# Kernel tuning notes

Measured on AMD Instinct MI355X. Metric: run time of the kernel, lower is better.

The kernel has to match this reference:

```python
import jax, jax.numpy as jnp
import numpy as np

B = 64            # batch of graphs
E = 8978          # edge-simplices per graph (nodes of the Hodge-1 graph)
E2 = E // 2       # after Graclus pair-pooling
K = 4             # Laguerre polynomial order
DEG = 16          # avg degree of the (edge-)adjacency
SLOPE = 0.33      # LeakyReLU negative slope
EPS = 1e-5        # BatchNorm eps


def _make_edges(rng, b, n, deg):
    # block-diagonal batched edge list: each graph only connects within itself
    offs = np.repeat(np.arange(b, dtype=np.int64) * n, n * deg)
    dst = np.tile(np.repeat(np.arange(n, dtype=np.int64), deg), b) + offs
    src = rng.integers(0, n, size=b * n * deg) + offs
    return np.stack([src, dst]).astype(np.int32)


def setup_inputs() -> dict:
    rng = np.random.default_rng(0)
    ks = jax.random.split(jax.random.key(0), 12)
    N1 = B * E
    ei1 = _make_edges(rng, B, E, DEG)
    ei2 = _make_edges(rng, B, E2, DEG)
    return {
        "x_s": jax.random.normal(ks[0], (N1, 1), jnp.float32),
        "edge_index_s": jnp.asarray(ei1),
        "edge_weight_s": jax.random.uniform(ks[1], (ei1.shape[1],), jnp.float32) * (2.0 / DEG),
        "edge_index_s1": jnp.asarray(ei2),
        "edge_weight_s1": jax.random.uniform(ks[2], (ei2.shape[1],), jnp.float32) * (2.0 / DEG),
        "W0": jax.random.normal(ks[3], (K, 1, 32), jnp.float32) * 0.3,
        "b0": jnp.zeros((32,), jnp.float32),
        "g0": jnp.ones((32,), jnp.float32),
        "be0": jnp.zeros((32,), jnp.float32),
        "W1": jax.random.normal(ks[4], (K, 32, 32), jnp.float32) * 0.1,
        "b1": jnp.zeros((32,), jnp.float32),
        "g1": jnp.ones((32,), jnp.float32),
        "be1": jnp.zeros((32,), jnp.float32),
        "W2": jax.random.normal(ks[5], (K, 32, 1), jnp.float32) * 0.1,
        "b2": jnp.zeros((1,), jnp.float32),
        "g2": jnp.ones((1,), jnp.float32),
        "be2": jnp.zeros((1,), jnp.float32),
        "lin1_W": jax.random.normal(ks[6], (E2, 256), jnp.float32) * 0.02,
        "lin1_b": jnp.zeros((256,), jnp.float32),
        "bn1_g": jnp.ones((256,), jnp.float32),
        "bn1_b": jnp.zeros((256,), jnp.float32),
        "lin2_W": jax.random.normal(ks[7], (256, 128), jnp.float32) * 0.06,
        "lin2_b": jnp.zeros((128,), jnp.float32),
        "bn2_g": jnp.ones((128,), jnp.float32),
        "bn2_b": jnp.zeros((128,), jnp.float32),
        "lin3_W": jax.random.normal(ks[8], (128, 1), jnp.float32) * 0.09,
        "lin3_b": jnp.zeros((1,), jnp.float32),
    }


def _laguerre_layer(x, src, dst, ew, W, b, gamma, beta, n):
    """HodgeLaguerreConv (K-order Laguerre recurrence over sparse L) + BatchNorm + LeakyReLU."""
    def matvec(v):  # (L v)[i] = sum_j w_ij v[j]
        return jax.ops.segment_sum(ew[:, None] * v[src], dst, num_segments=n)
    Tp = x                      # L_0(L) x = x
    out = Tp @ W[0]
    Tc = x - matvec(x)          # L_1(L) x = x - L x
    out = out + Tc @ W[1]
    for k in range(1, K - 1):   # L_{k+1} = ((2k+1-L) L_k - k L_{k-1}) / (k+1)
        Tn = ((2 * k + 1) * Tc - matvec(Tc) - k * Tp) / (k + 1)
        out = out + Tn @ W[k + 1]
        Tp, Tc = Tc, Tn
    out = out + b
    out = gamma * (out - out.mean(0)) * jax.lax.rsqrt(out.var(0) + EPS) + beta
    return jnp.where(out > 0, out, SLOPE * out)


def _bn(h, g, b):
    return g * (h - h.mean(0)) * jax.lax.rsqrt(h.var(0) + EPS) + b


def reference(x_s, edge_index_s, edge_weight_s, edge_index_s1, edge_weight_s1,
              W0, b0, g0, be0, W1, b1, g1, be1, W2, b2, g2, be2,
              lin1_W, lin1_b, bn1_g, bn1_b, lin2_W, lin2_b, bn2_g, bn2_b,
              lin3_W, lin3_b):
    N1, N2 = B * E, B * E2
    x = _laguerre_layer(x_s, edge_index_s[0], edge_index_s[1], edge_weight_s,
                        W0, b0, g0, be0, N1)
    # Graclus pooling: merge matched node pairs by max over features
    x = x.reshape(B, E2, 2, x.shape[-1]).max(axis=2).reshape(N2, -1)
    x = _laguerre_layer(x, edge_index_s1[0], edge_index_s1[1], edge_weight_s1,
                        W1, b1, g1, be1, N2)
    x = _laguerre_layer(x, edge_index_s1[0], edge_index_s1[1], edge_weight_s1,
                        W2, b2, g2, be2, N2)
    x = x.reshape(B, E2)        # last conv has 1 channel
    h = jax.nn.relu(_bn(x @ lin1_W + lin1_b, bn1_g, bn1_b))
    h = jax.nn.relu(_bn(h @ lin2_W + lin2_b, bn2_g, bn2_b))
    return h @ lin3_W + lin3_b  # [B, num_classes=1]
```

## Files before the change

kernel.cpp:

```cpp
#include <hip/hip_runtime.h>
#include <cstdint>

#define SLOPE 0.33f

static constexpr int B_   = 64;
static constexpr int E1_  = 8978;
static constexpr int E2_  = 4489;
static constexpr int N1_  = B_ * E1_;
static constexpr int N2_  = B_ * E2_;
static constexpr int DEG_ = 16;
static constexpr int SLC1_ = 1123;
static constexpr int SLC2_ = 562;
static constexpr double EPS_ = 1e-5;

typedef unsigned short u16;
typedef unsigned int   u32;

__device__ __forceinline__ float lrelu(float v) { return v > 0.f ? v : SLOPE * v; }
__device__ __forceinline__ float dot4(float4 a, float4 b) {
  return a.x * b.x + a.y * b.y + a.z * b.z + a.w * b.w;
}
__device__ __forceinline__ void gacc(float4& acc, float wgt, const float4& gv) {
  acc.x += wgt * gv.x; acc.y += wgt * gv.y; acc.z += wgt * gv.z; acc.w += wgt * gv.w;
}

template<int NPG>
__device__ __forceinline__ void comp_idx(const int* __restrict__ src, int node,
    u16* __restrict__ out) {
  int gbase = (node / NPG) * NPG;
  const int4* s4 = (const int4*)(src + (size_t)node * DEG_);
  int4 a = s4[0], b = s4[1], c = s4[2], d = s4[3];
  uint4 o0, o1;
  o0.x = (u32)(a.x - gbase) | ((u32)(a.y - gbase) << 16);
  o0.y = (u32)(a.z - gbase) | ((u32)(a.w - gbase) << 16);
  o0.z = (u32)(b.x - gbase) | ((u32)(b.y - gbase) << 16);
  o0.w = (u32)(b.z - gbase) | ((u32)(b.w - gbase) << 16);
  o1.x = (u32)(c.x - gbase) | ((u32)(c.y - gbase) << 16);
  o1.y = (u32)(c.z - gbase) | ((u32)(c.w - gbase) << 16);
  o1.z = (u32)(d.x - gbase) | ((u32)(d.y - gbase) << 16);
  o1.w = (u32)(d.z - gbase) | ((u32)(d.w - gbase) << 16);
  uint4* op = (uint4*)(out + (size_t)node * DEG_);
  op[0] = o0; op[1] = o1;
}

__global__ __launch_bounds__(256) void k_prep_all(const int* __restrict__ src1,
    const int* __restrict__ src2, const float* __restrict__ W1,
    u16* __restrict__ lsrc1, u16* __restrict__ lsrc2, float* __restrict__ qb) {
  int blk = blockIdx.x;
  if (blk < 2245) {
    int node = blk * 256 + threadIdx.x;
    if (node < N1_) comp_idx<E1_>(src1, node, lsrc1);
  } else if (blk < 3368) {
    int node = (blk - 2245) * 256 + threadIdx.x;
    if (node < N2_) comp_idx<E2_>(src2, node, lsrc2);
  } else {
    int idx = (blk - 3368) * 256 + threadIdx.x;
    if (idx < 4096) {
      int e = idx & 3, rr = (idx >> 2) & 3, qq = (idx >> 4) & 7, oq = idx >> 7;
      int j = oq >> 3, c = (oq & 7) * 4 + rr, in = 4 * qq + e;
      float k0, k1, k2, k3;
      if (j == 0)      { k0 = 0.f; k1 = 0.f; k2 = 0.f;  k3 = -1.f / 6.f; }
      else if (j == 1) { k0 = 0.f; k1 = 0.f; k2 = 0.5f; k3 = 1.5f; }
      else if (j == 2) { k0 = 0.f; k1 = -1.f; k2 = -2.f; k3 = -3.f; }
      else             { k0 = 1.f; k1 = 1.f; k2 = 1.f;  k3 = 1.f; }
      const float* wp = W1 + in * 32 + c;
      qb[idx] = k0 * wp[0] + k1 * wp[1024] + k2 * wp[2048] + k3 * wp[3072];
    }
  }
}

#define GATHER1(dst, sv, si_, w4_)                                              \
  {                                                                             \
    uint4 A_ = si_[0], Bq_ = si_[1];                                            \
    float4 w_;                                                                  \
    w_ = w4_[0];                                                                \
    dst += w_.x * sv[A_.x & 0xFFFFu] + w_.y * sv[A_.x >> 16]                    \
         + w_.z * sv[A_.y & 0xFFFFu] + w_.w * sv[A_.y >> 16];                   \
    w_ = w4_[1];                                                                \
    dst += w_.x * sv[A_.z & 0xFFFFu] + w_.y * sv[A_.z >> 16]                    \
         + w_.z * sv[A_.w & 0xFFFFu] + w_.w * sv[A_.w >> 16];                   \
    w_ = w4_[2];                                                                \
    dst += w_.x * sv[Bq_.x & 0xFFFFu] + w_.y * sv[Bq_.x >> 16]                  \
         + w_.z * sv[Bq_.y & 0xFFFFu] + w_.w * sv[Bq_.y >> 16];                 \
    w_ = w4_[3];                                                                \
    dst += w_.x * sv[Bq_.z & 0xFFFFu] + w_.y * sv[Bq_.z >> 16]                  \
         + w_.z * sv[Bq_.w & 0xFFFFu] + w_.w * sv[Bq_.w >> 16];                 \
  }

__global__ __launch_bounds__(512) void k0_mv1(const float* __restrict__ x,
    const u16* __restrict__ lsrc, const float* __restrict__ ew, float* __restrict__ T1) {
  __shared__ float sx[E1_];
  int g = blockIdx.x >> 3, q = blockIdx.x & 7;
  int gbase = g * E1_;
  for (int j = threadIdx.x; j < E1_; j += 512) sx[j] = x[gbase + j];
  __syncthreads();
  int start = q * SLC1_, end = min(start + SLC1_, E1_);
  for (int i = start + (int)threadIdx.x; i < end; i += 512) {
    int node = gbase + i;
    const uint4* si = (const uint4*)(lsrc + (size_t)node * DEG_);
    const float4* w4 = (const float4*)(ew + (size_t)node * DEG_);
    float acc = 0.f;
    GATHER1(acc, sx, si, w4);
    T1[node] = sx[i] - acc;
  }
}

__global__ __launch_bounds__(512) void k0_mv2(const float* __restrict__ x,
    const u16* __restrict__ lsrc, const float* __restrict__ ew,
    const float* __restrict__ T1, float* __restrict__ T2) {
  __shared__ float sT[E1_];
  int g = blockIdx.x >> 3, q = blockIdx.x & 7;
  int gbase = g * E1_;
  for (int j = threadIdx.x; j < E1_; j += 512) sT[j] = T1[gbase + j];
  __syncthreads();
  int start = q * SLC1_, end = min(start + SLC1_, E1_);
  for (int i = start + (int)threadIdx.x; i < end; i += 512) {
    int node = gbase + i;
    const uint4* si = (const uint4*)(lsrc + (size_t)node * DEG_);
    const float4* w4 = (const float4*)(ew + (size_t)node * DEG_);
    float acc = 0.f;
    GATHER1(acc, sT, si, w4);
    T2[node] = (3.f * sT[i] - acc - x[node]) * 0.5f;
  }
}

__global__ __launch_bounds__(512) void k0_mv3(const float* __restrict__ x,
    const u16* __restrict__ lsrc, const float* __restrict__ ew,
    const float* __restrict__ T1, const float* __restrict__ T2,
    float* __restrict__ T3, double* mom) {
  __shared__ float sT[E1_];
  __shared__ double sred[8 * 14];
  int g = blockIdx.x >> 3, q = blockIdx.x & 7;
  int gbase = g * E1_;
  for (int j = threadIdx.x; j < E1_; j += 512) sT[j] = T2[gbase + j];
  __syncthreads();
  double m[14];
#pragma unroll
  for (int j = 0; j < 14; ++j) m[j] = 0.0;
  int start = q * SLC1_, end = min(start + SLC1_, E1_);
  for (int i = start + (int)threadIdx.x; i < end; i += 512) {
    int node = gbase + i;
    const uint4* si = (const uint4*)(lsrc + (size_t)node * DEG_);
    const float4* w4 = (const float4*)(ew + (size_t)node * DEG_);
    float acc = 0.f;
    GATHER1(acc, sT, si, w4);
    float t1 = T1[node];
    float t2 = sT[i];
    float t3 = (5.f * t2 - acc - 2.f * t1) * (1.f / 3.f);
    T3[node] = t3;
    double d0 = x[node], d1 = t1, d2 = t2, d3 = t3;
    m[0] += d0; m[1] += d1; m[2] += d2; m[3] += d3;
    m[4] += d0 * d0; m[5] += d0 * d1; m[6] += d0 * d2; m[7] += d0 * d3;
    m[8] += d1 * d1; m[9] += d1 * d2; m[10] += d1 * d3;
    m[11] += d2 * d2; m[12] += d2 * d3; m[13] += d3 * d3;
  }
  int lane = threadIdx.x & 63, wid = threadIdx.x >> 6;
#pragma unroll
  for (int j = 0; j < 14; ++j) {
    double v = m[j];
    for (int o = 32; o; o >>= 1) v += __shfl_down(v, o);
    if (lane == 0) sred[wid * 14 + j] = v;
  }
  __syncthreads();
  if (threadIdx.x < 14) {
    double s = 0.0;
#pragma unroll
    for (int w = 0; w < 8; ++w) s += sred[w * 14 + threadIdx.x];
    atomicAdd(&mom[threadIdx.x], s);
  }
}

__global__ void k0_params(const double* __restrict__ mom, const float* __restrict__ W0,
    const float* __restrict__ g0, const float* __restrict__ be0,
    float* __restrict__ scale0, float* __restrict__ shiftE0, float* __restrict__ scW0) {
  int c = threadIdx.x;
  if (c >= 32) return;
  double inv = 1.0 / (double)N1_;
  double mm[4];
#pragma unroll
  for (int k = 0; k < 4; ++k) mm[k] = mom[k] * inv;
  double M[4][4];
  M[0][0] = mom[4] * inv;  M[0][1] = mom[5] * inv;  M[0][2] = mom[6] * inv;  M[0][3] = mom[7] * inv;
  M[1][1] = mom[8] * inv;  M[1][2] = mom[9] * inv;  M[1][3] = mom[10] * inv;
  M[2][2] = mom[11] * inv; M[2][3] = mom[12] * inv; M[3][3] = mom[13] * inv;
  M[1][0] = M[0][1]; M[2][0] = M[0][2]; M[3][0] = M[0][3];
  M[2][1] = M[1][2]; M[3][1] = M[1][3]; M[3][2] = M[2][3];
  double w[4];
#pragma unroll
  for (int k = 0; k < 4; ++k) w[k] = W0[k * 32 + c];
  double mean = 0.0;
#pragma unroll
  for (int k = 0; k < 4; ++k) mean += w[k] * mm[k];
  double e2 = 0.0;
#pragma unroll
  for (int k = 0; k < 4; ++k)
#pragma unroll
    for (int l = 0; l < 4; ++l) e2 += M[k][l] * w[k] * w[l];
  double var = e2 - mean * mean;
  double sc = (double)g0[c] / sqrt(var + EPS_);
  scale0[c] = (float)sc;
  shiftE0[c] = (float)((double)be0[c] - sc * mean);
#pragma unroll
  for (int k = 0; k < 4; ++k) scW0[c * 4 + k] = (float)(sc * w[k]);
}

__global__ __launch_bounds__(256) void k_poolproj(const float* __restrict__ x,
    const float* __restrict__ T1, const float* __restrict__ T2, const float* __restrict__ T3,
    const float* __restrict__ scW0, const float* __restrict__ shiftE0,
    const float* __restrict__ qb, float4* __restrict__ P4) {
  int r = blockIdx.x * 256 + threadIdx.x;
  if (r >= N2_) return;
  const float4* wt = (const float4*)scW0;
  float4 xr[8];
  {
    int b = r / E2_, j = r - b * E2_;
    int ga = b * E1_ + 2 * j;
    float2 xv = *(const float2*)(x + ga);
    float2 t1 = *(const float2*)(T1 + ga);
    float2 t2 = *(const float2*)(T2 + ga);
    float2 t3 = *(const float2*)(T3 + ga);
#pragma unroll
    for (int c8 = 0; c8 < 8; ++c8) {
      float4 o;
#pragma unroll
      for (int e = 0; e < 4; ++e) {
        int c = c8 * 4 + e;
        float4 w = wt[c];
        float sh = shiftE0[c];
        float da = w.x * xv.x + w.y * t1.x + w.z * t2.x + w.w * t3.x + sh;
        float db = w.x * xv.y + w.y * t1.y + w.z * t2.y + w.w * t3.y + sh;
        float v = fmaxf(lrelu(da), lrelu(db));
        if (e == 0) o.x = v; else if (e == 1) o.y = v; else if (e == 2) o.z = v; else o.w = v;
      }
      xr[c8] = o;
    }
  }
  const float4* qb4 = (const float4*)qb;
  for (int oq = 0; oq < 32; ++oq) {
    float4 acc = {0.f, 0.f, 0.f, 0.f};
#pragma unroll
    for (int qq = 0; qq < 8; ++qq) {
      const float4* wq = qb4 + (oq * 8 + qq) * 4;
      float4 w0 = wq[0], w1 = wq[1], w2 = wq[2], w3 = wq[3];
      float4 xq = xr[qq];
      acc.x += dot4(xq, w0);
      acc.y += dot4(xq, w1);
      acc.z += dot4(xq, w2);
      acc.w += dot4(xq, w3);
    }
    P4[(size_t)oq * N2_ + r] = acc;
  }
}

__global__ __launch_bounds__(1024) void k1_chain(const float4* __restrict__ P4,
    float4* __restrict__ O4, const u16* __restrict__ lsrc,
    const float* __restrict__ ew, double* st) {
  __shared__ float4 bA[E2_], bB[E2_];
  __shared__ float sacc[8];
  int v = (blockIdx.x & 7) * 64 + (blockIdx.x >> 3);
  int g = v >> 3, cg = v & 7;
  int gbase = g * E2_;
  int tid = threadIdx.x;
  if (tid < 8) sacc[tid] = 0.f;
  {
    const float4* sp = P4 + (size_t)cg * N2_ + gbase;
    for (int i = tid; i < E2_; i += 1024) bA[i] = sp[i];
  }
  float4* cur = bA;
  float4* nxt = bB;
  for (int s = 1; s <= 3; ++s) {
    __syncthreads();
    const float4* selfp = P4 + (size_t)(s * 8 + cg) * N2_ + gbase;
    for (int n = tid; n < E2_; n += 1024) {
      const uint4* si = (const uint4*)(lsrc + (size_t)(gbase + n) * DEG_);
      const float4* w4 = (const float4*)(ew + (size_t)(gbase + n) * DEG_);
      uint4 A = si[0], Bq = si[1];
      float4 acc = selfp[n];
      float4 w;
      w = w4[0];
      gacc(acc, w.x, cur[A.x & 0xFFFFu]); gacc(acc, w.y, cur[A.x >> 16]);
      gacc(acc, w.z, cur[A.y & 0xFFFFu]); gacc(acc, w.w, cur[A.y >> 16]);
      w = w4[1];
      gacc(acc, w.x, cur[A.z & 0xFFFFu]); gacc(acc, w.y, cur[A.z >> 16]);
      gacc(acc, w.z, cur[A.w & 0xFFFFu]); gacc(acc, w.w, cur[A.w >> 16]);
      w = w4[2];
      gacc(acc, w.x, cur[Bq.x & 0xFFFFu]); gacc(acc, w.y, cur[Bq.x >> 16]);
      gacc(acc, w.z, cur[Bq.y & 0xFFFFu]); gacc(acc, w.w, cur[Bq.y >> 16]);
      w = w4[3];
      gacc(acc, w.x, cur[Bq.z & 0xFFFFu]); gacc(acc, w.y, cur[Bq.z >> 16]);
      gacc(acc, w.z, cur[Bq.w & 0xFFFFu]); gacc(acc, w.w, cur[Bq.w >> 16]);
      nxt[n] = acc;
    }
    float4* t = cur; cur = nxt; nxt = t;
  }
  __syncthreads();
  float4* op = O4 + (size_t)cg * N2_ + gbase;
  float4 s1 = {0.f, 0.f, 0.f, 0.f}, s2 = {0.f, 0.f, 0.f, 0.f};
  for (int n = tid; n < E2_; n += 1024) {
    float4 vv = cur[n];
    op[n] = vv;
    s1.x += vv.x; s1.y += vv.y; s1.z += vv.z; s1.w += vv.w;
    s2.x += vv.x * vv.x; s2.y += vv.y * vv.y; s2.z += vv.z * vv.z; s2.w += vv.w * vv.w;
  }
  for (int o = 32; o; o >>= 1) {
    s1.x += __shfl_down(s1.x, o); s1.y += __shfl_down(s1.y, o);
    s1.z += __shfl_down(s1.z, o); s1.w += __shfl_down(s1.w, o);
    s2.x += __shfl_down(s2.x, o); s2.y += __shfl_down(s2.y, o);
    s2.z += __shfl_down(s2.z, o); s2.w += __shfl_down(s2.w, o);
  }
  if ((tid & 63) == 0) {
    atomicAdd(&sacc[0], s1.x); atomicAdd(&sacc[1], s1.y);
    atomicAdd(&sacc[2], s1.z); atomicAdd(&sacc[3], s1.w);
    atomicAdd(&sacc[4], s2.x); atomicAdd(&sacc[5], s2.y);
    atomicAdd(&sacc[6], s2.z); atomicAdd(&sacc[7], s2.w);
  }
  __syncthreads();
  if (tid < 4) {
    int ch = cg * 4 + tid;
    atomicAdd(&st[ch], (double)sacc[tid]);
    atomicAdd(&st[32 + ch], (double)sacc[4 + tid]);
  }
}

__global__ void k1_params(const double* __restrict__ sum, const double* __restrict__ sq,
    const float* __restrict__ g1, const float* __restrict__ be1,
    float* __restrict__ scale1, float* __restrict__ shiftE1) {
  int c = threadIdx.x;
  if (c >= 32) return;
  double mean = sum[c] / (double)N2_;
  double var = sq[c] / (double)N2_ - mean * mean;
  double sc = (double)g1[c] / sqrt(var + EPS_);
  scale1[c] = (float)sc;
  shiftE1[c] = (float)((double)be1[c] - sc * mean);
}

__global__ __launch_bounds__(256) void k2_proj(const float* __restrict__ X,
    const float* __restrict__ W2, const float* __restrict__ scale1,
    const float* __restrict__ shiftE1,
    float* __restrict__ u0, float* __restrict__ u1,
    float* __restrict__ u2, float* __restrict__ u3) {
  __shared__ float qv[4][32];
  __shared__ float fsc[32], fsh[32];
  int tid = threadIdx.x;
  if (tid < 128) {
    int cp = tid & 31, j = tid >> 5;
    float w0 = W2[cp], w1 = W2[32 + cp], w2 = W2[64 + cp], w3 = W2[96 + cp];
    float q;
    if (j == 0)      q = w0 + w1 + w2 + w3;
    else if (j == 1) q = -w1 - 2.f * w2 - 3.f * w3;
    else if (j == 2) q = 0.5f * w2 + 1.5f * w3;
    else             q = -w3 * (1.f / 6.f);
    qv[j][cp] = q;
  }
  if (tid < 32) { fsc[tid] = scale1[tid]; fsh[tid] = shiftE1[tid]; }
  __syncthreads();
  int node = blockIdx.x * 256 + tid;
  if (node >= N2_) return;
  const float4* xf = (const float4*)X;
  float a0 = 0.f, a1 = 0.f, a2 = 0.f, a3 = 0.f;
#pragma unroll
  for (int t = 0; t < 8; ++t) {
    float4 v = xf[(size_t)t * N2_ + node];
    float f0 = lrelu(fsc[4 * t] * v.x + fsh[4 * t]);
    float f1 = lrelu(fsc[4 * t + 1] * v.y + fsh[4 * t + 1]);
    float f2_ = lrelu(fsc[4 * t + 2] * v.z + fsh[4 * t + 2]);
    float f3 = lrelu(fsc[4 * t + 3] * v.w + fsh[4 * t + 3]);
    a0 += f0 * qv[0][4 * t] + f1 * qv[0][4 * t + 1] + f2_ * qv[0][4 * t + 2] + f3 * qv[0][4 * t + 3];
    a1 += f0 * qv[1][4 * t] + f1 * qv[1][4 * t + 1] + f2_ * qv[1][4 * t + 2] + f3 * qv[1][4 * t + 3];
    a2 += f0 * qv[2][4 * t] + f1 * qv[2][4 * t + 1] + f2_ * qv[2][4 * t + 2] + f3 * qv[2][4 * t + 3];
    a3 += f0 * qv[3][4 * t] + f1 * qv[3][4 * t + 1] + f2_ * qv[3][4 * t + 2] + f3 * qv[3][4 * t + 3];
  }
  u0[node] = a0; u1[node] = a1; u2[node] = a2; u3[node] = a3;
}

__global__ __launch_bounds__(512) void k2_step(const float* __restrict__ z,
    const u16* __restrict__ lsrc, const float* __restrict__ ew,
    const float* __restrict__ u, float* __restrict__ zo,
    int do_stats, double* st2) {
  __shared__ float sz[E2_];
  __shared__ double sred[8][2];
  int g = blockIdx.x >> 3, q = blockIdx.x & 7;
  int gbase = g * E2_;
  for (int j = threadIdx.x; j < E2_; j += 512) sz[j] = z[gbase + j];
  __syncthreads();
  int start = q * SLC2_, end = min(start + SLC2_, E2_);
  double aS = 0.0, aQ = 0.0;
  for (int i = start + (int)threadIdx.x; i < end; i += 512) {
    int node = gbase + i;
    const uint4* si = (const uint4*)(lsrc + (size_t)node * DEG_);
    const float4* w4 = (const float4*)(ew + (size_t)node * DEG_);
    float acc = 0.f;
    GATHER1(acc, sz, si, w4);
    float val = u[node] + acc;
    zo[node] = val;
    if (do_stats) { aS += val; aQ += (double)val * (double)val; }
  }
  if (do_stats) {
    int lane = threadIdx.x & 63, wid = threadIdx.x >> 6;
    for (int o = 32; o; o >>= 1) { aS += __shfl_down(aS, o); aQ += __shfl_down(aQ, o); }
    if (lane == 0) { sred[wid][0] = aS; sred[wid][1] = aQ; }
    __syncthreads();
    if (threadIdx.x == 0) {
      double s = 0.0, qq = 0.0;
#pragma unroll
      for (int w = 0; w < 8; ++w) { s += sred[w][0]; qq += sred[w][1]; }
      atomicAdd(&st2[0], s); atomicAdd(&st2[1], qq);
    }
  }
}

__global__ void k2_params(const double* __restrict__ st2, const float* __restrict__ g2,
    const float* __restrict__ be2, float* __restrict__ p ) {
  if (threadIdx.x != 0) return;
  double mean = st2[0] / (double)N2_;
  double var = st2[1] / (double)N2_ - mean * mean;
  double sc = (double)g2[0] / sqrt(var + EPS_);
  p[128] = (float)sc;
  p[129] = (float)((double)be2[0] - sc * mean);
}

__global__ __launch_bounds__(256) void k3_gemm1(const float* __restrict__ out2,
    const float* __restrict__ lin1W, const float* __restrict__ p, float* h1pre) {
  __shared__ float f2v[8][144];
  float sc = p[128], sh = p[129];
  int bs = blockIdx.x & 7, rs = blockIdx.x >> 3;
  int b0 = bs * 8;
  int r0 = rs * 141;
  int nr = min(141, E2_ - r0);
  int c = threadIdx.x;
#pragma unroll
  for (int b = 0; b < 8; ++b)
    for (int j = c; j < 144; j += 256)
      f2v[b][j] = (j < nr) ? lrelu(sc * out2[(b0 + b) * E2_ + r0 + j] + sh) : 0.f;
  __syncthreads();
  float acc[8];
#pragma unroll
  for (int b = 0; b < 8; ++b) acc[b] = 0.f;
  int nr4 = nr & ~3;
  int j = 0;
  for (; j < nr4; j += 4) {
    const float* wp = lin1W + (size_t)(r0 + j) * 256 + c;
    float w0 = wp[0], w1 = wp[256], w2 = wp[512], w3 = wp[768];
#pragma unroll
    for (int b = 0; b < 8; ++b) {
      float4 f = *(const float4*)&f2v[b][j];
      acc[b] += f.x * w0 + f.y * w1 + f.z * w2 + f.w * w3;
    }
  }
  for (; j < nr; ++j) {
    float w = lin1W[(size_t)(r0 + j) * 256 + c];
#pragma unroll
    for (int b = 0; b < 8; ++b) acc[b] += f2v[b][j] * w;
  }
#pragma unroll
  for (int b = 0; b < 8; ++b)
    atomicAdd(&h1pre[(b0 + b) * 256 + c], acc[b]);
}

__global__ __launch_bounds__(256) void k5_gemm2bn(const float* __restrict__ h1pre,
    const float* __restrict__ g, const float* __restrict__ be,
    const float* __restrict__ lin2W, float* __restrict__ h2pre) {
  __shared__ float sh1[64 * 257];
  __shared__ float sred[256];
  int c = blockIdx.x;
  int tid = threadIdx.x;
  for (int i = tid; i < 64 * 256; i += 256) {
    int b = i >> 8, cc = i & 255;
    sh1[b * 257 + cc] = h1pre[i];
  }
  __syncthreads();
  {
    int cc = tid;
    double s = 0.0, qd = 0.0;
    float vs[64];
#pragma unroll
    for (int b = 0; b < 64; ++b) { float v = sh1[b * 257 + cc]; vs[b] = v; s += v; qd += (double)v * v; }
    double mean = s / 64.0, var = qd / 64.0 - mean * mean;
    double scd = (double)g[cc] / sqrt(var + EPS_);
    double shd = (double)be[cc] - scd * mean;
#pragma unroll
    for (int b = 0; b < 64; ++b) {
      float y = (float)(scd * vs[b] + shd);
      sh1[b * 257 + cc] = y > 0.f ? y : 0.f;
    }
  }
  __syncthreads();
  int b = tid & 63, q = tid >> 6;
  float acc = 0.f;
  for (int r = q; r < 256; r += 4) acc += sh1[b * 257 + r] * lin2W[r * 128 + c];
  sred[tid] = acc;
  __syncthreads();
  if (tid < 64)
    h2pre[tid * 128 + c] = sred[tid] + sred[64 + tid] + sred[128 + tid] + sred[192 + tid];
}

__global__ __launch_bounds__(256) void k6_final(const float* __restrict__ h2pre,
    const float* __restrict__ g, const float* __restrict__ be,
    const float* __restrict__ W3, const float* __restrict__ b3, float* __restrict__ outp) {
  __shared__ float sh2[64 * 129];
  __shared__ float sred[256];
  int tid = threadIdx.x;
  if (tid < 128) {
    int c = tid;
    float vs[64];
    double s = 0.0, q = 0.0;
    for (int b = 0; b < 64; ++b) { float v = h2pre[b * 128 + c]; vs[b] = v; s += v; q += (double)v * v; }
    double mean = s / 64.0, var = q / 64.0 - mean * mean;
    double scd = (double)g[c] / sqrt(var + EPS_);
    double shd = (double)be[c] - scd * mean;
    for (int b = 0; b < 64; ++b) {
      float y = (float)(scd * vs[b] + shd);
      sh2[b * 129 + c] = y > 0.f ? y : 0.f;
    }
  }
  __syncthreads();
  int b = tid & 63, q = tid >> 6;
  float acc = 0.f;
  for (int r = q; r < 128; r += 4) acc += sh2[b * 129 + r] * W3[r];
  sred[tid] = acc;
  __syncthreads();
  if (tid < 64)
    outp[tid] = sred[tid] + sred[64 + tid] + sred[128 + tid] + sred[192 + tid] + b3[0];
}

extern "C" void kernel_launch(void* const* d_in, const int* in_sizes, int n_in,
                              void* d_out, int out_size, void* d_ws, size_t ws_size,
                              hipStream_t stream) {
  const float* x    = (const float*)d_in[0];
  const int*   ei1  = (const int*)d_in[1];
  const float* ew1  = (const float*)d_in[2];
  const int*   ei2  = (const int*)d_in[3];
  const float* ew2  = (const float*)d_in[4];
  const float* W0   = (const float*)d_in[5];
  const float* g0   = (const float*)d_in[7];
  const float* be0  = (const float*)d_in[8];
  const float* W1   = (const float*)d_in[9];
  const float* g1   = (const float*)d_in[11];
  const float* be1  = (const float*)d_in[12];
  const float* W2   = (const float*)d_in[13];
  const float* g2   = (const float*)d_in[15];
  const float* be2  = (const float*)d_in[16];
  const float* lin1W = (const float*)d_in[17];
  const float* bn1g = (const float*)d_in[19];
  const float* bn1b = (const float*)d_in[20];
  const float* lin2W = (const float*)d_in[21];
  const float* bn2g = (const float*)d_in[23];
  const float* bn2b = (const float*)d_in[24];
  const float* lin3W = (const float*)d_in[25];
  const float* lin3b = (const float*)d_in[26];

  char* ws = (char*)d_ws;
  double* stats  = (double*)ws;
  float*  params = (float*)(ws + 1024);
  float*  h1pre  = (float*)(ws + 4096);
  float*  h2pre  = (float*)(ws + 4096 + 131072);
  float*  qb     = (float*)(ws + 196608);
  float*  Treg   = (float*)(ws + 262144);
  float* T1_0 = Treg;
  float* T2_0 = Treg + N1_;
  float* T3_0 = Treg + 2 * (size_t)N1_;
  float* u0   = Treg;
  float* u1   = Treg + (size_t)N2_;
  float* u2   = Treg + 2 * (size_t)N2_;
  float* u3   = Treg + 3 * (size_t)N2_;
  float* zA   = Treg + 4 * (size_t)N2_;
  float* out2 = Treg + 5 * (size_t)N2_;
  float*  big = (float*)(ws + 262144 + 3 * (size_t)N1_ * 4);
  float* bufA = big;
  float* Pbuf = big + 32 * (size_t)N2_;
  u16* lsrc1 = (u16*)Pbuf;
  u16* lsrc2 = (u16*)bufA;

  hipMemsetAsync(stats, 0, 80 * sizeof(double), stream);
  hipMemsetAsync(h1pre, 0, 65536, stream);

  k_prep_all<<<3384, 256, 0, stream>>>(ei1, ei2, W1, lsrc1, lsrc2, qb);

  k0_mv1<<<512, 512, 0, stream>>>(x, lsrc1, ew1, T1_0);
  k0_mv2<<<512, 512, 0, stream>>>(x, lsrc1, ew1, T1_0, T2_0);
  k0_mv3<<<512, 512, 0, stream>>>(x, lsrc1, ew1, T1_0, T2_0, T3_0, stats);
  k0_params<<<1, 32, 0, stream>>>(stats, W0, g0, be0, params, params + 32, params + 160);

  k_poolproj<<<(N2_ + 255) / 256, 256, 0, stream>>>(x, T1_0, T2_0, T3_0,
                                                    params + 160, params + 32, qb, (float4*)Pbuf);

  k1_chain<<<512, 1024, 0, stream>>>((const float4*)Pbuf, (float4*)Pbuf, lsrc2, ew2, stats + 14);
  k1_params<<<1, 32, 0, stream>>>(stats + 14, stats + 46, g1, be1, params + 64, params + 96);

  k2_proj<<<(N2_ + 255) / 256, 256, 0, stream>>>(Pbuf, W2, params + 64, params + 96,
                                                 u0, u1, u2, u3);
  k2_step<<<512, 512, 0, stream>>>(u3, lsrc2, ew2, u2, zA, 0, nullptr);
  k2_step<<<512, 512, 0, stream>>>(zA, lsrc2, ew2, u1, u3, 0, nullptr);
  k2_step<<<512, 512, 0, stream>>>(u3, lsrc2, ew2, u0, out2, 1, stats + 78);
  k2_params<<<1, 64, 0, stream>>>(stats + 78, g2, be2, params);

  k3_gemm1<<<256, 256, 0, stream>>>(out2, lin1W, params, h1pre);
  k5_gemm2bn<<<128, 256, 0, stream>>>(h1pre, bn1g, bn1b, lin2W, h2pre);
  k6_final<<<1, 256, 0, stream>>>(h2pre, bn2g, bn2b, lin3W, lin3b, (float*)d_out);
}
```

Measured before the change: 470.6 us.

## Fuse per-graph Laguerre matvec chains into single-block-per-graph kernels

```diff
diff --git a/kernel.cpp b/kernel.cpp
--- a/kernel.cpp
+++ b/kernel.cpp
@@ -9,8 +9,6 @@
 static constexpr int N1_  = B_ * E1_;
 static constexpr int N2_  = B_ * E2_;
 static constexpr int DEG_ = 16;
-static constexpr int SLC1_ = 1123;
-static constexpr int SLC2_ = 562;
 static constexpr double EPS_ = 1e-5;
 
 typedef unsigned short u16;
@@ -87,68 +85,52 @@
          + w_.z * sv[Bq_.w & 0xFFFFu] + w_.w * sv[Bq_.w >> 16];                 \
   }
 
-__global__ __launch_bounds__(512) void k0_mv1(const float* __restrict__ x,
-    const u16* __restrict__ lsrc, const float* __restrict__ ew, float* __restrict__ T1) {
-  __shared__ float sx[E1_];
-  int g = blockIdx.x >> 3, q = blockIdx.x & 7;
+__global__ __launch_bounds__(1024) void k0_chain(const float* __restrict__ x,
+    const u16* __restrict__ lsrc, const float* __restrict__ ew,
+    float* __restrict__ T1, float* __restrict__ T2, float* __restrict__ T3,
+    double* mom) {
+  __shared__ float sx[E1_], s1[E1_], s2[E1_];
+  __shared__ double sred[16 * 14];
+  int g = blockIdx.x;
   int gbase = g * E1_;
-  for (int j = threadIdx.x; j < E1_; j += 512) sx[j] = x[gbase + j];
-  __syncthreads();
-  int start = q * SLC1_, end = min(start + SLC1_, E1_);
-  for (int i = start + (int)threadIdx.x; i < end; i += 512) {
+  int tid = threadIdx.x;
+  for (int j = tid; j < E1_; j += 1024) sx[j] = x[gbase + j];
+  __syncthreads();
+  for (int i = tid; i < E1_; i += 1024) {
     int node = gbase + i;
     const uint4* si = (const uint4*)(lsrc + (size_t)node * DEG_);
     const float4* w4 = (const float4*)(ew + (size_t)node * DEG_);
     float acc = 0.f;
     GATHER1(acc, sx, si, w4);
-    T1[node] = sx[i] - acc;
-  }
-}
-
-__global__ __launch_bounds__(512) void k0_mv2(const float* __restrict__ x,
-    const u16* __restrict__ lsrc, const float* __restrict__ ew,
-    const float* __restrict__ T1, float* __restrict__ T2) {
-  __shared__ float sT[E1_];
-  int g = blockIdx.x >> 3, q = blockIdx.x & 7;
-  int gbase = g * E1_;
-  for (int j = threadIdx.x; j < E1_; j += 512) sT[j] = T1[gbase + j];
-  __syncthreads();
-  int start = q * SLC1_, end = min(start + SLC1_, E1_);
-  for (int i = start + (int)threadIdx.x; i < end; i += 512) {
+    float t1 = sx[i] - acc;
+    s1[i] = t1;
+    T1[node] = t1;
+  }
+  __syncthreads();
+  for (int i = tid; i < E1_; i += 1024) {
     int node = gbase + i;
     const uint4* si = (const uint4*)(lsrc + (size_t)node * DEG_);
     const float4* w4 = (const float4*)(ew + (size_t)node * DEG_);
     float acc = 0.f;
-    GATHER1(acc, sT, si, w4);
-    T2[node] = (3.f * sT[i] - acc - x[node]) * 0.5f;
-  }
-}
-
-__global__ __launch_bounds__(512) void k0_mv3(const float* __restrict__ x,
-    const u16* __restrict__ lsrc, const float* __restrict__ ew,
-    const float* __restrict__ T1, const float* __restrict__ T2,
-    float* __restrict__ T3, double* mom) {
-  __shared__ float sT[E1_];
-  __shared__ double sred[8 * 14];
-  int g = blockIdx.x >> 3, q = blockIdx.x & 7;
-  int gbase = g * E1_;
-  for (int j = threadIdx.x; j < E1_; j += 512) sT[j] = T2[gbase + j];
+    GATHER1(acc, s1, si, w4);
+    float t2 = (3.f * s1[i] - acc - sx[i]) * 0.5f;
+    s2[i] = t2;
+    T2[node] = t2;
+  }
   __syncthreads();
   double m[14];
 #pragma unroll
   for (int j = 0; j < 14; ++j) m[j] = 0.0;
-  int start = q * SLC1_, end = min(start + SLC1_, E1_);
-  for (int i = start + (int)threadIdx.x; i < end; i += 512) {
+  for (int i = tid; i < E1_; i += 1024) {
     int node = gbase + i;
     const uint4* si = (const uint4*)(lsrc + (size_t)node * DEG_);
     const float4* w4 = (const float4*)(ew + (size_t)node * DEG_);
     float acc = 0.f;
-    GATHER1(acc, sT, si, w4);
-    float t1 = T1[node];
-    float t2 = sT[i];
+    GATHER1(acc, s2, si, w4);
+    float t1 = s1[i], t2 = s2[i];
     float t3 = (5.f * t2 - acc - 2.f * t1) * (1.f / 3.f);
     T3[node] = t3;
-    double d0 = x[node], d1 = t1, d2 = t2, d3 = t3;
+    double d0 = sx[i], d1 = t1, d2 = t2, d3 = t3;
     m[0] += d0; m[1] += d1; m[2] += d2; m[3] += d3;
     m[4] += d0 * d0; m[5] += d0 * d1; m[6] += d0 * d2; m[7] += d0 * d3;
     m[8] += d1 * d1; m[9] += d1 * d2; m[10] += d1 * d3;
@@ -162,11 +144,11 @@
     if (lane == 0) sred[wid * 14 + j] = v;
   }
   __syncthreads();
-  if (threadIdx.x < 14) {
+  if (tid < 14) {
     double s = 0.0;
 #pragma unroll
-    for (int w = 0; w < 8; ++w) s += sred[w * 14 + threadIdx.x];
-    atomicAdd(&mom[threadIdx.x], s);
+    for (int w = 0; w < 16; ++w) s += sred[w * 14 + tid];
+    atomicAdd(&mom[tid], s);
   }
 }
 
@@ -334,13 +316,16 @@
   shiftE1[c] = (float)((double)be1[c] - sc * mean);
 }
 
-__global__ __launch_bounds__(256) void k2_proj(const float* __restrict__ X,
+__global__ __launch_bounds__(1024) void k2_chain(const float* __restrict__ X,
     const float* __restrict__ W2, const float* __restrict__ scale1,
-    const float* __restrict__ shiftE1,
-    float* __restrict__ u0, float* __restrict__ u1,
-    float* __restrict__ u2, float* __restrict__ u3) {
+    const float* __restrict__ shiftE1, const u16* __restrict__ lsrc,
+    const float* __restrict__ ew, float* __restrict__ out2, double* st2) {
+  __shared__ float zA[E2_], zB[E2_];
   __shared__ float qv[4][32];
   __shared__ float fsc[32], fsh[32];
+  __shared__ double sred[16][2];
+  int g = blockIdx.x;
+  int gbase = g * E2_;
   int tid = threadIdx.x;
   if (tid < 128) {
     int cp = tid & 31, j = tid >> 5;
@@ -354,58 +339,80 @@
   }
   if (tid < 32) { fsc[tid] = scale1[tid]; fsh[tid] = shiftE1[tid]; }
   __syncthreads();
-  int node = blockIdx.x * 256 + tid;
-  if (node >= N2_) return;
+  float u0r[5], u1r[5], u2r[5];
   const float4* xf = (const float4*)X;
-  float a0 = 0.f, a1 = 0.f, a2 = 0.f, a3 = 0.f;
-#pragma unroll
-  for (int t = 0; t < 8; ++t) {
-    float4 v = xf[(size_t)t * N2_ + node];
-    float f0 = lrelu(fsc[4 * t] * v.x + fsh[4 * t]);
-    float f1 = lrelu(fsc[4 * t + 1] * v.y + fsh[4 * t + 1]);
-    float f2_ = lrelu(fsc[4 * t + 2] * v.z + fsh[4 * t + 2]);
-    float f3 = lrelu(fsc[4 * t + 3] * v.w + fsh[4 * t + 3]);
-    a0 += f0 * qv[0][4 * t] + f1 * qv[0][4 * t + 1] + f2_ * qv[0][4 * t + 2] + f3 * qv[0][4 * t + 3];
-    a1 += f0 * qv[1][4 * t] + f1 * qv[1][4 * t + 1] + f2_ * qv[1][4 * t + 2] + f3 * qv[1][4 * t + 3];
-    a2 += f0 * qv[2][4 * t] + f1 * qv[2][4 * t + 1] + f2_ * qv[2][4 * t + 2] + f3 * qv[2][4 * t + 3];
-    a3 += f0 * qv[3][4 * t] + f1 * qv[3][4 * t + 1] + f2_ * qv[3][4 * t + 2] + f3 * qv[3][4 * t + 3];
-  }
-  u0[node] = a0; u1[node] = a1; u2[node] = a2; u3[node] = a3;
-}
-
-__global__ __launch_bounds__(512) void k2_step(const float* __restrict__ z,
-    const u16* __restrict__ lsrc, const float* __restrict__ ew,
-    const float* __restrict__ u, float* __restrict__ zo,
-    int do_stats, double* st2) {
-  __shared__ float sz[E2_];
-  __shared__ double sred[8][2];
-  int g = blockIdx.x >> 3, q = blockIdx.x & 7;
-  int gbase = g * E2_;
-  for (int j = threadIdx.x; j < E2_; j += 512) sz[j] = z[gbase + j];
-  __syncthreads();
-  int start = q * SLC2_, end = min(start + SLC2_, E2_);
+#pragma unroll
+  for (int k = 0; k < 5; ++k) {
+    int n = tid + k * 1024;
+    if (n < E2_) {
+      float a0 = 0.f, a1 = 0.f, a2 = 0.f, a3 = 0.f;
+#pragma unroll
+      for (int t = 0; t < 8; ++t) {
+        float4 v = xf[(size_t)t * N2_ + gbase + n];
+        float f0 = lrelu(fsc[4 * t] * v.x + fsh[4 * t]);
+        float f1 = lrelu(fsc[4 * t + 1] * v.y + fsh[4 * t + 1]);
+        float f2_ = lrelu(fsc[4 * t + 2] * v.z + fsh[4 * t + 2]);
+        float f3 = lrelu(fsc[4 * t + 3] * v.w + fsh[4 * t + 3]);
+        a0 += f0 * qv[0][4 * t] + f1 * qv[0][4 * t + 1] + f2_ * qv[0][4 * t + 2] + f3 * qv[0][4 * t + 3];
+        a1 += f0 * qv[1][4 * t] + f1 * qv[1][4 * t + 1] + f2_ * qv[1][4 * t + 2] + f3 * qv[1][4 * t + 3];
+        a2 += f0 * qv[2][4 * t] + f1 * qv[2][4 * t + 1] + f2_ * qv[2][4 * t + 2] + f3 * qv[2][4 * t + 3];
+        a3 += f0 * qv[3][4 * t] + f1 * qv[3][4 * t + 1] + f2_ * qv[3][4 * t + 2] + f3 * qv[3][4 * t + 3];
+      }
+      u0r[k] = a0; u1r[k] = a1; u2r[k] = a2;
+      zA[n] = a3;
+    }
+  }
+  __syncthreads();
+#pragma unroll
+  for (int k = 0; k < 5; ++k) {
+    int n = tid + k * 1024;
+    if (n < E2_) {
+      int node = gbase + n;
+      const uint4* si = (const uint4*)(lsrc + (size_t)node * DEG_);
+      const float4* w4 = (const float4*)(ew + (size_t)node * DEG_);
+      float acc = 0.f;
+      GATHER1(acc, zA, si, w4);
+      zB[n] = u2r[k] + acc;
+    }
+  }
+  __syncthreads();
+#pragma unroll
+  for (int k = 0; k < 5; ++k) {
+    int n = tid + k * 1024;
+    if (n < E2_) {
+      int node = gbase + n;
+      const uint4* si = (const uint4*)(lsrc + (size_t)node * DEG_);
+      const float4* w4 = (const float4*)(ew + (size_t)node * DEG_);
+      float acc = 0.f;
+      GATHER1(acc, zB, si, w4);
+      zA[n] = u1r[k] + acc;
+    }
+  }
+  __syncthreads();
   double aS = 0.0, aQ = 0.0;
-  for (int i = start + (int)threadIdx.x; i < end; i += 512) {
-    int node = gbase + i;
-    const uint4* si = (const uint4*)(lsrc + (size_t)node * DEG_);
-    const float4* w4 = (const float4*)(ew + (size_t)node * DEG_);
-    float acc = 0.f;
-    GATHER1(acc, sz, si, w4);
-    float val = u[node] + acc;
-    zo[node] = val;
-    if (do_stats) { aS += val; aQ += (double)val * (double)val; }
-  }
-  if (do_stats) {
-    int lane = threadIdx.x & 63, wid = threadIdx.x >> 6;
-    for (int o = 32; o; o >>= 1) { aS += __shfl_down(aS, o); aQ += __shfl_down(aQ, o); }
-    if (lane == 0) { sred[wid][0] = aS; sred[wid][1] = aQ; }
-    __syncthreads();
-    if (threadIdx.x == 0) {
-      double s = 0.0, qq = 0.0;
-#pragma unroll
-      for (int w = 0; w < 8; ++w) { s += sred[w][0]; qq += sred[w][1]; }
-      atomicAdd(&st2[0], s); atomicAdd(&st2[1], qq);
-    }
+#pragma unroll
+  for (int k = 0; k < 5; ++k) {
+    int n = tid + k * 1024;
+    if (n < E2_) {
+      int node = gbase + n;
+      const uint4* si = (const uint4*)(lsrc + (size_t)node * DEG_);
+      const float4* w4 = (const float4*)(ew + (size_t)node * DEG_);
+      float acc = 0.f;
+      GATHER1(acc, zA, si, w4);
+      float val = u0r[k] + acc;
+      out2[node] = val;
+      aS += val; aQ += (double)val * (double)val;
+    }
+  }
+  int lane = tid & 63, wid = tid >> 6;
+  for (int o = 32; o; o >>= 1) { aS += __shfl_down(aS, o); aQ += __shfl_down(aQ, o); }
+  if (lane == 0) { sred[wid][0] = aS; sred[wid][1] = aQ; }
+  __syncthreads();
+  if (tid == 0) {
+    double s = 0.0, qq = 0.0;
+#pragma unroll
+    for (int w = 0; w < 16; ++w) { s += sred[w][0]; qq += sred[w][1]; }
+    atomicAdd(&st2[0], s); atomicAdd(&st2[1], qq);
   }
 }
 
@@ -559,11 +566,6 @@
   float* T1_0 = Treg;
   float* T2_0 = Treg + N1_;
   float* T3_0 = Treg + 2 * (size_t)N1_;
-  float* u0   = Treg;
-  float* u1   = Treg + (size_t)N2_;
-  float* u2   = Treg + 2 * (size_t)N2_;
-  float* u3   = Treg + 3 * (size_t)N2_;
-  float* zA   = Treg + 4 * (size_t)N2_;
   float* out2 = Treg + 5 * (size_t)N2_;
   float*  big = (float*)(ws + 262144 + 3 * (size_t)N1_ * 4);
   float* bufA = big;
@@ -576,9 +578,7 @@
 
   k_prep_all<<<3384, 256, 0, stream>>>(ei1, ei2, W1, lsrc1, lsrc2, qb);
 
-  k0_mv1<<<512, 512, 0, stream>>>(x, lsrc1, ew1, T1_0);
-  k0_mv2<<<512, 512, 0, stream>>>(x, lsrc1, ew1, T1_0, T2_0);
-  k0_mv3<<<512, 512, 0, stream>>>(x, lsrc1, ew1, T1_0, T2_0, T3_0, stats);
+  k0_chain<<<64, 1024, 0, stream>>>(x, lsrc1, ew1, T1_0, T2_0, T3_0, stats);
   k0_params<<<1, 32, 0, stream>>>(stats, W0, g0, be0, params, params + 32, params + 160);
 
   k_poolproj<<<(N2_ + 255) / 256, 256, 0, stream>>>(x, T1_0, T2_0, T3_0,
@@ -587,11 +587,8 @@
   k1_chain<<<512, 1024, 0, stream>>>((const float4*)Pbuf, (float4*)Pbuf, lsrc2, ew2, stats + 14);
   k1_params<<<1, 32, 0, stream>>>(stats + 14, stats + 46, g1, be1, params + 64, params + 96);
 
-  k2_proj<<<(N2_ + 255) / 256, 256, 0, stream>>>(Pbuf, W2, params + 64, params + 96,
-                                                 u0, u1, u2, u3);
-  k2_step<<<512, 512, 0, stream>>>(u3, lsrc2, ew2, u2, zA, 0, nullptr);
-  k2_step<<<512, 512, 0, stream>>>(zA, lsrc2, ew2, u1, u3, 0, nullptr);
-  k2_step<<<512, 512, 0, stream>>>(u3, lsrc2, ew2, u0, out2, 1, stats + 78);
+  k2_chain<<<64, 1024, 0, stream>>>(Pbuf, W2, params + 64, params + 96,
+                                    lsrc2, ew2, out2, stats + 78);
   k2_params<<<1, 64, 0, stream>>>(stats + 78, g2, be2, params);
 
   k3_gemm1<<<256, 256, 0, stream>>>(out2, lin1W, params, h1pre);
```

Result: slower. 485.6 us (+3.2%).
